# Kernel optimization log

Measured on AMD Instinct MI355X. Metric: run time of the kernel, lower is better.

## Reference

```python
import jax, jax.numpy as jnp
import numpy as np

N_DOMAINS = 8
LN_EPS = 1e-5


def setup_inputs() -> dict:
    key = jax.random.key(0)
    ks = jax.random.split(key, 4)
    N, D_IN, D_HID, D_OUT = 32768, 256, 1024, 256
    x = jax.random.normal(ks[0], (N, D_IN), dtype=jnp.float32)
    domain_types = jax.random.randint(ks[1], (N,), 0, N_DOMAINS, dtype=jnp.int32)
    # Per-domain MLP parameters (8 independent experts)
    W1 = jax.random.normal(ks[2], (N_DOMAINS, D_IN, D_HID), dtype=jnp.float32) * (1.0 / np.sqrt(D_IN))
    b1 = jnp.zeros((N_DOMAINS, D_HID), dtype=jnp.float32)
    gamma = jnp.ones((N_DOMAINS, D_HID), dtype=jnp.float32)
    beta = jnp.zeros((N_DOMAINS, D_HID), dtype=jnp.float32)
    W2 = jax.random.normal(ks[3], (N_DOMAINS, D_HID, D_OUT), dtype=jnp.float32) * (1.0 / np.sqrt(D_HID))
    b2 = jnp.zeros((N_DOMAINS, D_OUT), dtype=jnp.float32)
    return {"x": x, "domain_types": domain_types, "W1": W1, "b1": b1,
            "gamma": gamma, "beta": beta, "W2": W2, "b2": b2}


def _expert_mlp(x, W1d, b1d, gd, bd, W2d, b2d):
    # Linear -> LayerNorm -> ReLU -> (Dropout: identity at eval) -> Linear
    h = x @ W1d + b1d                       # [N, hid]
    mu = jnp.mean(h, axis=-1, keepdims=True)
    var = jnp.mean(jnp.square(h - mu), axis=-1, keepdims=True)
    h = (h - mu) * jax.lax.rsqrt(var + LN_EPS) * gd + bd
    h = jax.nn.relu(h)
    return h @ W2d + b2d                    # [N, out]


def reference(x, domain_types, W1, b1, gamma, beta, W2, b2):
    # output dim == x.shape[-1] (as in the torch code: zeros(batch, x.shape[-1]))
    out = jnp.zeros((x.shape[0], x.shape[-1]), dtype=x.dtype)
    for d in range(N_DOMAINS):  # small fixed expert loop (static MoE dispatch)
        y = _expert_mlp(x, W1[d], b1[d], gamma[d], beta[d], W2[d], b2[d])
        mask = (domain_types == d)[:, None]
        out = jnp.where(mask, y, out)
    return out
```

## Files before the change

### kernel.cpp

```cpp
#include <hip/hip_runtime.h>
#include <hip/hip_bf16.h>


#define ND 8
#define NROWS 32768
#define DIN 256
#define DHID 1024
#define DOUT 256
#define RPT 64
#define MPAD64 33280
#define NT64 520

typedef short short8 __attribute__((ext_vector_type(8)));
typedef float floatx4 __attribute__((ext_vector_type(4)));

__device__ __forceinline__ unsigned short f2bf(float f) {
    unsigned u = __builtin_bit_cast(unsigned, f);
    unsigned r = u + 0x7fff + ((u >> 16) & 1);
    return (unsigned short)(r >> 16);
}

__global__ void transpose_bf16(const float* __restrict__ in,
                               unsigned short* __restrict__ out,
                               int R, int C) {
    __shared__ float t[32][33];
    const int z = blockIdx.z;
    const int c0 = blockIdx.x * 32, r0 = blockIdx.y * 32;
    const int tx = threadIdx.x & 31, ty = threadIdx.x >> 5;
    const float* src = in + (size_t)z * R * C;
    unsigned short* dst = out + (size_t)z * R * C;
#pragma unroll
    for (int i = 0; i < 32; i += 8)
        t[ty + i][tx] = src[(size_t)(r0 + ty + i) * C + c0 + tx];
    __syncthreads();
#pragma unroll
    for (int i = 0; i < 32; i += 8)
        dst[(size_t)(c0 + ty + i) * R + r0 + tx] = f2bf(t[tx][ty + i]);
}

__global__ void zero_init(int* __restrict__ perm, int* __restrict__ cnt) {
    int i = blockIdx.x * 256 + threadIdx.x;
    if (i < MPAD64) perm[i] = -1;
    if (i < 16) cnt[i] = 0;
}

__global__ void histo(const int* __restrict__ dt, int* __restrict__ counts) {
    __shared__ int lc[ND];
    if (threadIdx.x < ND) lc[threadIdx.x] = 0;
    __syncthreads();
    int i = blockIdx.x * 256 + threadIdx.x;
    atomicAdd(&lc[dt[i]], 1);
    __syncthreads();
    if (threadIdx.x < ND) atomicAdd(&counts[threadIdx.x], lc[threadIdx.x]);
}

__global__ void make_meta(const int* __restrict__ counts, int* __restrict__ cursors,
                          int2* __restrict__ meta) {
    __shared__ int base[ND], ntc[ND];
    const int t = threadIdx.x;
    if (t == 0) {
        int off = 0;
        for (int d = 0; d < ND; d++) {
            base[d] = off;
            ntc[d] = (counts[d] + 63) >> 6;
            cursors[d] = off;
            off += ntc[d] << 6;
        }
    }
    __syncthreads();
    for (int i = t; i < NT64; i += 64) {
        int2 m = make_int2(-1, 0);
#pragma unroll
        for (int d = 0; d < ND; d++) {
            const int ti = i - (base[d] >> 6);
            if (ti >= 0 && ti < ntc[d]) m = make_int2(d, base[d] + (ti << 6));
        }
        meta[i] = m;
    }
}

__global__ __launch_bounds__(256)
void assign_pos(const int* __restrict__ dt, int* __restrict__ cursors,
                int* __restrict__ perm) {
    __shared__ int lcnt[ND];
    __shared__ int lbase[ND];
    const int tid = threadIdx.x;
    if (tid < ND) lcnt[tid] = 0;
    __syncthreads();
    const int r = blockIdx.x * 256 + tid;
    const int d = dt[r];
    const int myrank = atomicAdd(&lcnt[d], 1);
    __syncthreads();
    if (tid < ND && lcnt[tid] > 0)
        lbase[tid] = atomicAdd(&cursors[tid], lcnt[tid]);
    __syncthreads();
    perm[lbase[d] + myrank] = r;
}

__global__ __launch_bounds__(512, 2)
void fused_mlp(const float* __restrict__ x,
               const unsigned short* __restrict__ W1T,
               const float* __restrict__ b1,
               const float* __restrict__ gamma,
               const float* __restrict__ beta,
               const unsigned short* __restrict__ W2T,
               const float* __restrict__ b2,
               const int2* __restrict__ meta,
               const int* __restrict__ perm,
               float* __restrict__ out) {
    const int bid = (int)blockIdx.x;
    const int swz = (bid & 7) * (NT64 >> 3) + (bid >> 3);
    const int2 md = meta[swz];
    const int dom = md.x;
    if (dom < 0) return;
    const int m0 = md.y;

    __shared__ unsigned short Hs[RPT * DHID];
    __shared__ float red[1024];
    unsigned short* Axs = Hs;

    const int tid = threadIdx.x;
    const int lane = tid & 63;
    const int w = tid >> 6;
    const int l15 = lane & 15;
    const int q = lane >> 4;

    {
        const int row = tid >> 3;
        const int c8 = tid & 7;
        const int orig = perm[m0 + row];
        const int sw = (row & 7) << 3;
        if (orig >= 0) {
            const float4* src = (const float4*)(x + (size_t)orig * DIN);
#pragma unroll
            for (int it = 0; it < 8; ++it) {
                const int c = it * 8 + c8;
                const float4 v = src[c];
                ushort4 o;
                o.x = f2bf(v.x); o.y = f2bf(v.y); o.z = f2bf(v.z); o.w = f2bf(v.w);
                *(ushort4*)&Axs[(row * DIN + c * 4) ^ sw] = o;
            }
        } else {
            const ushort4 z = {0, 0, 0, 0};
#pragma unroll
            for (int it = 0; it < 8; ++it) {
                const int c = it * 8 + c8;
                *(ushort4*)&Axs[(row * DIN + c * 4) ^ sw] = z;
            }
        }
    }

    const int n0w = w * 128;
    const unsigned short* B1p = W1T + (size_t)dom * DHID * DIN
                              + (size_t)(n0w + l15) * DIN + q * 8;
    short8 bA[8], bB[8];
#pragma unroll
    for (int j = 0; j < 8; ++j)
        bA[j] = *(const short8*)(B1p + (size_t)j * 16 * DIN);

    __syncthreads();

    floatx4 acc[4][8];
#pragma unroll
    for (int i = 0; i < 4; ++i)
#pragma unroll
        for (int j = 0; j < 8; ++j) acc[i][j] = 0.f;

#pragma unroll
    for (int t = 0; t < 8; ++t) {
        const int k0 = t * 32;
        short8* bc = (t & 1) ? bB : bA;
        short8* bn = (t & 1) ? bA : bB;
        if (t < 7) {
#pragma unroll
            for (int j = 0; j < 8; ++j)
                bn[j] = *(const short8*)(B1p + (size_t)j * 16 * DIN + (k0 + 32));
        }
        short8 a[4];
#pragma unroll
        for (int i = 0; i < 4; ++i) {
            const int row = i * 16 + l15;
            a[i] = *(const short8*)&Axs[(row * DIN + k0 + q * 8) ^ ((row & 7) << 3)];
        }
        __builtin_amdgcn_s_setprio(1);
#pragma unroll
        for (int i = 0; i < 4; ++i)
#pragma unroll
            for (int j = 0; j < 8; ++j)
                acc[i][j] = __builtin_amdgcn_mfma_f32_16x16x32_bf16(a[i], bc[j], acc[i][j], 0, 0, 0);
        __builtin_amdgcn_s_setprio(0);
    }

    float b1v[8], gv[8], bv[8];
#pragma unroll
    for (int j = 0; j < 8; ++j) {
        const int col = n0w + j * 16 + l15;
        b1v[j] = b1[dom * DHID + col];
        gv[j]  = gamma[dom * DHID + col];
        bv[j]  = beta[dom * DHID + col];
    }
#pragma unroll
    for (int i = 0; i < 4; ++i)
#pragma unroll
        for (int j = 0; j < 8; ++j)
#pragma unroll
            for (int r = 0; r < 4; ++r) acc[i][j][r] += b1v[j];

#pragma unroll
    for (int i = 0; i < 4; ++i)
#pragma unroll
        for (int r = 0; r < 4; ++r) {
            float s = 0.f, s2 = 0.f;
#pragma unroll
            for (int j = 0; j < 8; ++j) {
                const float v = acc[i][j][r];
                s += v; s2 += v * v;
            }
#pragma unroll
            for (int o = 8; o; o >>= 1) {
                s  += __shfl_xor(s, o, 64);
                s2 += __shfl_xor(s2, o, 64);
            }
            if (l15 == 0) {
                const int row = i * 16 + q * 4 + r;
                red[w * 64 + row]       = s;
                red[512 + w * 64 + row] = s2;
            }
        }
    __syncthreads();
    if (tid < 64) {
        float s = 0.f, s2 = 0.f;
#pragma unroll
        for (int ww = 0; ww < 8; ++ww) {
            s  += red[ww * 64 + tid];
            s2 += red[512 + ww * 64 + tid];
        }
        const float mu  = s * (1.f / 1024.f);
        const float var = fmaxf(s2 * (1.f / 1024.f) - mu * mu, 0.f);
        red[tid]      = mu;
        red[64 + tid] = rsqrtf(var + 1e-5f);
    }
    __syncthreads();

#pragma unroll
    for (int i = 0; i < 4; ++i)
#pragma unroll
        for (int r = 0; r < 4; ++r) {
            const int row = i * 16 + q * 4 + r;
            const float mu   = red[row];
            const float rstd = red[64 + row];
            const int sw = (row & 7) << 3;
#pragma unroll
            for (int j = 0; j < 8; ++j) {
                const int col = n0w + j * 16 + l15;
                const float v = fmaxf((acc[i][j][r] - mu) * rstd * gv[j] + bv[j], 0.f);
                Hs[(row * DHID + col) ^ sw] = f2bf(v);
            }
        }
    __syncthreads();

    floatx4 acc2[4][2];
#pragma unroll
    for (int i = 0; i < 4; ++i) { acc2[i][0] = 0.f; acc2[i][1] = 0.f; }

    const int c0w = w * 32;
    const unsigned short* B2p = W2T + (size_t)dom * DOUT * DHID
                              + (size_t)(c0w + l15) * DHID + q * 8;
    short8 cA[2], cB[2];
#pragma unroll
    for (int jj = 0; jj < 2; ++jj)
        cA[jj] = *(const short8*)(B2p + (size_t)jj * 16 * DHID);

    for (int t = 0; t < 32; t += 2) {
        const int k0 = t * 32;
        if (t + 1 < 32) {
#pragma unroll
            for (int jj = 0; jj < 2; ++jj)
                cB[jj] = *(const short8*)(B2p + (size_t)jj * 16 * DHID + (k0 + 32));
        }
        {
            short8 a[4];
#pragma unroll
            for (int ii = 0; ii < 4; ++ii) {
                const int row = ii * 16 + l15;
                a[ii] = *(const short8*)&Hs[(row * DHID + k0 + q * 8) ^ ((row & 7) << 3)];
            }
            __builtin_amdgcn_s_setprio(1);
#pragma unroll
            for (int ii = 0; ii < 4; ++ii)
#pragma unroll
                for (int jj = 0; jj < 2; ++jj)
                    acc2[ii][jj] = __builtin_amdgcn_mfma_f32_16x16x32_bf16(a[ii], cA[jj], acc2[ii][jj], 0, 0, 0);
            __builtin_amdgcn_s_setprio(0);
        }
        if (t + 2 < 32) {
#pragma unroll
            for (int jj = 0; jj < 2; ++jj)
                cA[jj] = *(const short8*)(B2p + (size_t)jj * 16 * DHID + (k0 + 64));
        }
        {
            short8 a[4];
#pragma unroll
            for (int ii = 0; ii < 4; ++ii) {
                const int row = ii * 16 + l15;
                a[ii] = *(const short8*)&Hs[(row * DHID + k0 + 32 + q * 8) ^ ((row & 7) << 3)];
            }
            __builtin_amdgcn_s_setprio(1);
#pragma unroll
            for (int ii = 0; ii < 4; ++ii)
#pragma unroll
                for (int jj = 0; jj < 2; ++jj)
                    acc2[ii][jj] = __builtin_amdgcn_mfma_f32_16x16x32_bf16(a[ii], cB[jj], acc2[ii][jj], 0, 0, 0);
            __builtin_amdgcn_s_setprio(0);
        }
    }

    float b2v[2];
#pragma unroll
    for (int jj = 0; jj < 2; ++jj)
        b2v[jj] = b2[dom * DOUT + c0w + jj * 16 + l15];
#pragma unroll
    for (int ii = 0; ii < 4; ++ii)
#pragma unroll
        for (int r = 0; r < 4; ++r) {
            const int row = ii * 16 + q * 4 + r;
            const int orig = perm[m0 + row];
            if (orig < 0) continue;
#pragma unroll
            for (int jj = 0; jj < 2; ++jj)
                out[(size_t)orig * DOUT + c0w + jj * 16 + l15] = acc2[ii][jj][r] + b2v[jj];
        }
}

extern "C" void kernel_launch(void* const* d_in, const int* in_sizes, int n_in,
                              void* d_out, int out_size, void* d_ws, size_t ws_size,
                              hipStream_t stream) {
    const float* x = (const float*)d_in[0];
    const int* dt = (const int*)d_in[1];
    const float* W1 = (const float*)d_in[2];
    const float* b1 = (const float*)d_in[3];
    const float* gamma = (const float*)d_in[4];
    const float* beta = (const float*)d_in[5];
    const float* W2 = (const float*)d_in[6];
    const float* b2 = (const float*)d_in[7];
    float* out = (float*)d_out;

    char* ws = (char*)d_ws;
    size_t off = 0;
    auto take = [&](size_t nbytes) -> char* {
        char* p = ws + off;
        off = (off + nbytes + 255) & ~(size_t)255;
        return p;
    };
    unsigned short* W1T = (unsigned short*)take((size_t)ND * DHID * DIN * 2);
    unsigned short* W2T = (unsigned short*)take((size_t)ND * DOUT * DHID * 2);
    int* PERM = (int*)take(MPAD64 * 4);
    int* CNT  = (int*)take(64);
    int2* META = (int2*)take(NT64 * 8);
    (void)ws_size; (void)n_in; (void)in_sizes; (void)out_size;

    int* COUNTS = CNT;
    int* CURSORS = CNT + 8;

    transpose_bf16<<<dim3(DHID / 32, DIN / 32, ND), 256, 0, stream>>>(W1, W1T, DIN, DHID);
    transpose_bf16<<<dim3(DOUT / 32, DHID / 32, ND), 256, 0, stream>>>(W2, W2T, DHID, DOUT);
    zero_init<<<MPAD64 / 256, 256, 0, stream>>>(PERM, CNT);
    histo<<<NROWS / 256, 256, 0, stream>>>(dt, COUNTS);
    make_meta<<<1, 64, 0, stream>>>(COUNTS, CURSORS, META);
    assign_pos<<<NROWS / 256, 256, 0, stream>>>(dt, CURSORS, PERM);
    fused_mlp<<<NT64, 512, 0, stream>>>(x, W1T, b1, gamma, beta, W2T, b2, META, PERM, out);
}
```

Before: 235.3 us.

## Halve row tile to 32 and split hidden GEMM into two passes for occupancy

```diff
diff --git a/kernel.cpp b/kernel.cpp
--- a/kernel.cpp
+++ b/kernel.cpp
@@ -7,9 +7,9 @@
 #define DIN 256
 #define DHID 1024
 #define DOUT 256
-#define RPT 64
-#define MPAD64 33280
-#define NT64 520
+#define RPT 32
+#define MPAD32 33024
+#define NT32 1032
 
 typedef short short8 __attribute__((ext_vector_type(8)));
 typedef float floatx4 __attribute__((ext_vector_type(4)));
@@ -18,6 +18,10 @@
     unsigned u = __builtin_bit_cast(unsigned, f);
     unsigned r = u + 0x7fff + ((u >> 16) & 1);
     return (unsigned short)(r >> 16);
+}
+__device__ __forceinline__ float bf2f(unsigned short h) {
+    unsigned u = ((unsigned)h) << 16;
+    return __builtin_bit_cast(float, u);
 }
 
 __global__ void transpose_bf16(const float* __restrict__ in,
@@ -40,7 +44,7 @@
 
 __global__ void zero_init(int* __restrict__ perm, int* __restrict__ cnt) {
     int i = blockIdx.x * 256 + threadIdx.x;
-    if (i < MPAD64) perm[i] = -1;
+    if (i < MPAD32) perm[i] = -1;
     if (i < 16) cnt[i] = 0;
 }
 
@@ -62,18 +66,18 @@
         int off = 0;
         for (int d = 0; d < ND; d++) {
             base[d] = off;
-            ntc[d] = (counts[d] + 63) >> 6;
+            ntc[d] = (counts[d] + 31) >> 5;
             cursors[d] = off;
-            off += ntc[d] << 6;
-        }
-    }
-    __syncthreads();
-    for (int i = t; i < NT64; i += 64) {
+            off += ntc[d] << 5;
+        }
+    }
+    __syncthreads();
+    for (int i = t; i < NT32; i += 64) {
         int2 m = make_int2(-1, 0);
 #pragma unroll
         for (int d = 0; d < ND; d++) {
-            const int ti = i - (base[d] >> 6);
-            if (ti >= 0 && ti < ntc[d]) m = make_int2(d, base[d] + (ti << 6));
+            const int ti = i - (base[d] >> 5);
+            if (ti >= 0 && ti < ntc[d]) m = make_int2(d, base[d] + (ti << 5));
         }
         meta[i] = m;
     }
@@ -97,7 +101,7 @@
     perm[lbase[d] + myrank] = r;
 }
 
-__global__ __launch_bounds__(512, 2)
+__global__ __launch_bounds__(512, 4)
 void fused_mlp(const float* __restrict__ x,
                const unsigned short* __restrict__ W1T,
                const float* __restrict__ b1,
@@ -109,15 +113,15 @@
                const int* __restrict__ perm,
                float* __restrict__ out) {
     const int bid = (int)blockIdx.x;
-    const int swz = (bid & 7) * (NT64 >> 3) + (bid >> 3);
+    const int swz = (bid & 7) * (NT32 >> 3) + (bid >> 3);
     const int2 md = meta[swz];
     const int dom = md.x;
     if (dom < 0) return;
     const int m0 = md.y;
 
-    __shared__ unsigned short Hs[RPT * DHID];
-    __shared__ float red[1024];
-    unsigned short* Axs = Hs;
+    __shared__ __attribute__((aligned(16))) unsigned short Hs[RPT * DHID];
+    __shared__ __attribute__((aligned(16))) unsigned short Axs[RPT * DIN];
+    float* red = (float*)Axs;
 
     const int tid = threadIdx.x;
     const int lane = tid & 63;
@@ -125,16 +129,24 @@
     const int l15 = lane & 15;
     const int q = lane >> 4;
 
+    const unsigned short* W1d = W1T + (size_t)dom * DHID * DIN;
+    const unsigned short* Bp0 = W1d + (size_t)(w * 64 + l15) * DIN + q * 8;
+
+    short8 bA[4], bB[4];
+#pragma unroll
+    for (int j = 0; j < 4; ++j)
+        bA[j] = *(const short8*)(Bp0 + (size_t)j * 16 * DIN);
+
     {
-        const int row = tid >> 3;
-        const int c8 = tid & 7;
+        const int row = tid >> 4;
+        const int c16 = tid & 15;
         const int orig = perm[m0 + row];
         const int sw = (row & 7) << 3;
         if (orig >= 0) {
             const float4* src = (const float4*)(x + (size_t)orig * DIN);
 #pragma unroll
-            for (int it = 0; it < 8; ++it) {
-                const int c = it * 8 + c8;
+            for (int it = 0; it < 4; ++it) {
+                const int c = it * 16 + c16;
                 const float4 v = src[c];
                 ushort4 o;
                 o.x = f2bf(v.x); o.y = f2bf(v.y); o.z = f2bf(v.z); o.w = f2bf(v.w);
@@ -143,125 +155,109 @@
         } else {
             const ushort4 z = {0, 0, 0, 0};
 #pragma unroll
-            for (int it = 0; it < 8; ++it) {
-                const int c = it * 8 + c8;
+            for (int it = 0; it < 4; ++it) {
+                const int c = it * 16 + c16;
                 *(ushort4*)&Axs[(row * DIN + c * 4) ^ sw] = z;
             }
         }
     }
-
-    const int n0w = w * 128;
-    const unsigned short* B1p = W1T + (size_t)dom * DHID * DIN
-                              + (size_t)(n0w + l15) * DIN + q * 8;
-    short8 bA[8], bB[8];
-#pragma unroll
-    for (int j = 0; j < 8; ++j)
-        bA[j] = *(const short8*)(B1p + (size_t)j * 16 * DIN);
-
-    __syncthreads();
-
-    floatx4 acc[4][8];
-#pragma unroll
-    for (int i = 0; i < 4; ++i)
-#pragma unroll
-        for (int j = 0; j < 8; ++j) acc[i][j] = 0.f;
-
-#pragma unroll
-    for (int t = 0; t < 8; ++t) {
-        const int k0 = t * 32;
-        short8* bc = (t & 1) ? bB : bA;
-        short8* bn = (t & 1) ? bA : bB;
-        if (t < 7) {
-#pragma unroll
-            for (int j = 0; j < 8; ++j)
-                bn[j] = *(const short8*)(B1p + (size_t)j * 16 * DIN + (k0 + 32));
-        }
-        short8 a[4];
-#pragma unroll
-        for (int i = 0; i < 4; ++i) {
-            const int row = i * 16 + l15;
-            a[i] = *(const short8*)&Axs[(row * DIN + k0 + q * 8) ^ ((row & 7) << 3)];
-        }
-        __builtin_amdgcn_s_setprio(1);
-#pragma unroll
-        for (int i = 0; i < 4; ++i)
-#pragma unroll
-            for (int j = 0; j < 8; ++j)
-                acc[i][j] = __builtin_amdgcn_mfma_f32_16x16x32_bf16(a[i], bc[j], acc[i][j], 0, 0, 0);
-        __builtin_amdgcn_s_setprio(0);
-    }
-
-    float b1v[8], gv[8], bv[8];
-#pragma unroll
-    for (int j = 0; j < 8; ++j) {
-        const int col = n0w + j * 16 + l15;
-        b1v[j] = b1[dom * DHID + col];
-        gv[j]  = gamma[dom * DHID + col];
-        bv[j]  = beta[dom * DHID + col];
-    }
-#pragma unroll
-    for (int i = 0; i < 4; ++i)
-#pragma unroll
-        for (int j = 0; j < 8; ++j)
-#pragma unroll
-            for (int r = 0; r < 4; ++r) acc[i][j][r] += b1v[j];
-
-#pragma unroll
-    for (int i = 0; i < 4; ++i)
+    __syncthreads();
+
+    float sp[2][4], sp2[2][4];
+#pragma unroll
+    for (int i = 0; i < 2; ++i)
+#pragma unroll
+        for (int r = 0; r < 4; ++r) { sp[i][r] = 0.f; sp2[i][r] = 0.f; }
+
+#pragma unroll
+    for (int p = 0; p < 2; ++p) {
+        const int cb = p * 512 + w * 64;
+        const unsigned short* B1p = Bp0 + (size_t)(p * 512) * DIN;
+
+        floatx4 acc[2][4];
+#pragma unroll
+        for (int i = 0; i < 2; ++i)
+#pragma unroll
+            for (int j = 0; j < 4; ++j) acc[i][j] = 0.f;
+
+#pragma unroll
+        for (int t = 0; t < 8; ++t) {
+            const int k0 = t * 32;
+            short8* bc = (t & 1) ? bB : bA;
+            short8* bn = (t & 1) ? bA : bB;
+            if (t < 7) {
+#pragma unroll
+                for (int j = 0; j < 4; ++j)
+                    bn[j] = *(const short8*)(B1p + (size_t)j * 16 * DIN + (k0 + 32));
+            } else if (p == 0) {
+#pragma unroll
+                for (int j = 0; j < 4; ++j)
+                    bA[j] = *(const short8*)(Bp0 + (size_t)(512 + j * 16) * DIN);
+            }
+            short8 a[2];
+#pragma unroll
+            for (int i = 0; i < 2; ++i) {
+                const int row = i * 16 + l15;
+                a[i] = *(const short8*)&Axs[(row * DIN + k0 + q * 8) ^ ((row & 7) << 3)];
+            }
+            __builtin_amdgcn_s_setprio(1);
+#pragma unroll
+            for (int i = 0; i < 2; ++i)
+#pragma unroll
+                for (int j = 0; j < 4; ++j)
+                    acc[i][j] = __builtin_amdgcn_mfma_f32_16x16x32_bf16(a[i], bc[j], acc[i][j], 0, 0, 0);
+            __builtin_amdgcn_s_setprio(0);
+        }
+
+#pragma unroll
+        for (int j = 0; j < 4; ++j) {
+            const float b1v = b1[dom * DHID + cb + j * 16 + l15];
+#pragma unroll
+            for (int i = 0; i < 2; ++i)
+#pragma unroll
+                for (int r = 0; r < 4; ++r) acc[i][j][r] += b1v;
+        }
+#pragma unroll
+        for (int i = 0; i < 2; ++i)
+#pragma unroll
+            for (int r = 0; r < 4; ++r) {
+                float s = 0.f, s2 = 0.f;
+#pragma unroll
+                for (int j = 0; j < 4; ++j) {
+                    const float v = acc[i][j][r];
+                    s += v; s2 += v * v;
+                }
+                sp[i][r] += s; sp2[i][r] += s2;
+            }
+#pragma unroll
+        for (int i = 0; i < 2; ++i)
+#pragma unroll
+            for (int r = 0; r < 4; ++r) {
+                const int row = i * 16 + q * 4 + r;
+                const int sw = (row & 7) << 3;
+#pragma unroll
+                for (int j = 0; j < 4; ++j)
+                    Hs[(row * DHID + cb + j * 16 + l15) ^ sw] = f2bf(acc[i][j][r]);
+            }
+    }
+
+    __syncthreads();
+
+#pragma unroll
+    for (int i = 0; i < 2; ++i)
 #pragma unroll
         for (int r = 0; r < 4; ++r) {
-            float s = 0.f, s2 = 0.f;
-#pragma unroll
-            for (int j = 0; j < 8; ++j) {
-                const float v = acc[i][j][r];
-                s += v; s2 += v * v;
-            }
 #pragma unroll
             for (int o = 8; o; o >>= 1) {
-                s  += __shfl_xor(s, o, 64);
-                s2 += __shfl_xor(s2, o, 64);
+                sp[i][r]  += __shfl_xor(sp[i][r], o, 64);
+                sp2[i][r] += __shfl_xor(sp2[i][r], o, 64);
             }
             if (l15 == 0) {
                 const int row = i * 16 + q * 4 + r;
-                red[w * 64 + row]       = s;
-                red[512 + w * 64 + row] = s2;
-            }
-        }
-    __syncthreads();
-    if (tid < 64) {
-        float s = 0.f, s2 = 0.f;
-#pragma unroll
-        for (int ww = 0; ww < 8; ++ww) {
-            s  += red[ww * 64 + tid];
-            s2 += red[512 + ww * 64 + tid];
-        }
-        const float mu  = s * (1.f / 1024.f);
-        const float var = fmaxf(s2 * (1.f / 1024.f) - mu * mu, 0.f);
-        red[tid]      = mu;
-        red[64 + tid] = rsqrtf(var + 1e-5f);
-    }
-    __syncthreads();
-
-#pragma unroll
-    for (int i = 0; i < 4; ++i)
-#pragma unroll
-        for (int r = 0; r < 4; ++r) {
-            const int row = i * 16 + q * 4 + r;
-            const float mu   = red[row];
-            const float rstd = red[64 + row];
-            const int sw = (row & 7) << 3;
-#pragma unroll
-            for (int j = 0; j < 8; ++j) {
-                const int col = n0w + j * 16 + l15;
-                const float v = fmaxf((acc[i][j][r] - mu) * rstd * gv[j] + bv[j], 0.f);
-                Hs[(row * DHID + col) ^ sw] = f2bf(v);
-            }
-        }
-    __syncthreads();
-
-    floatx4 acc2[4][2];
-#pragma unroll
-    for (int i = 0; i < 4; ++i) { acc2[i][0] = 0.f; acc2[i][1] = 0.f; }
+                red[w * 32 + row]       = sp[i][r];
+                red[256 + w * 32 + row] = sp2[i][r];
+            }
+        }
 
     const int c0w = w * 32;
     const unsigned short* B2p = W2T + (size_t)dom * DOUT * DHID
@@ -271,6 +267,55 @@
     for (int jj = 0; jj < 2; ++jj)
         cA[jj] = *(const short8*)(B2p + (size_t)jj * 16 * DHID);
 
+    __syncthreads();
+    if (tid < 32) {
+        float s = 0.f, s2 = 0.f;
+#pragma unroll
+        for (int ww = 0; ww < 8; ++ww) {
+            s  += red[ww * 32 + tid];
+            s2 += red[256 + ww * 32 + tid];
+        }
+        const float mu  = s * (1.f / 1024.f);
+        const float var = fmaxf(s2 * (1.f / 1024.f) - mu * mu, 0.f);
+        red[512 + tid] = mu;
+        red[544 + tid] = rsqrtf(var + 1e-5f);
+    }
+    __syncthreads();
+
+    {
+        const float* gdp = gamma + dom * DHID;
+        const float* bdp = beta + dom * DHID;
+#pragma unroll
+        for (int kq = 0; kq < 8; ++kq) {
+            const int ch = tid + kq * 512;
+            const int row = ch >> 7;
+            const int c0 = (ch & 127) * 8;
+            const int idx = (row * DHID + c0) ^ ((row & 7) << 3);
+            short8 hv = *(short8*)&Hs[idx];
+            const float mu   = red[512 + row];
+            const float rstd = red[544 + row];
+            const float4 g0 = *(const float4*)(gdp + c0);
+            const float4 g1 = *(const float4*)(gdp + c0 + 4);
+            const float4 be0 = *(const float4*)(bdp + c0);
+            const float4 be1 = *(const float4*)(bdp + c0 + 4);
+            short8 o;
+            o[0] = (short)f2bf(fmaxf((bf2f((unsigned short)hv[0]) - mu) * rstd * g0.x + be0.x, 0.f));
+            o[1] = (short)f2bf(fmaxf((bf2f((unsigned short)hv[1]) - mu) * rstd * g0.y + be0.y, 0.f));
+            o[2] = (short)f2bf(fmaxf((bf2f((unsigned short)hv[2]) - mu) * rstd * g0.z + be0.z, 0.f));
+            o[3] = (short)f2bf(fmaxf((bf2f((unsigned short)hv[3]) - mu) * rstd * g0.w + be0.w, 0.f));
+            o[4] = (short)f2bf(fmaxf((bf2f((unsigned short)hv[4]) - mu) * rstd * g1.x + be1.x, 0.f));
+            o[5] = (short)f2bf(fmaxf((bf2f((unsigned short)hv[5]) - mu) * rstd * g1.y + be1.y, 0.f));
+            o[6] = (short)f2bf(fmaxf((bf2f((unsigned short)hv[6]) - mu) * rstd * g1.z + be1.z, 0.f));
+            o[7] = (short)f2bf(fmaxf((bf2f((unsigned short)hv[7]) - mu) * rstd * g1.w + be1.w, 0.f));
+            *(short8*)&Hs[idx] = o;
+        }
+    }
+    __syncthreads();
+
+    floatx4 acc2[2][2];
+#pragma unroll
+    for (int ii = 0; ii < 2; ++ii) { acc2[ii][0] = 0.f; acc2[ii][1] = 0.f; }
+
     for (int t = 0; t < 32; t += 2) {
         const int k0 = t * 32;
         if (t + 1 < 32) {
@@ -279,15 +324,15 @@
                 cB[jj] = *(const short8*)(B2p + (size_t)jj * 16 * DHID + (k0 + 32));
         }
         {
-            short8 a[4];
-#pragma unroll
-            for (int ii = 0; ii < 4; ++ii) {
+            short8 a[2];
+#pragma unroll
+            for (int ii = 0; ii < 2; ++ii) {
                 const int row = ii * 16 + l15;
                 a[ii] = *(const short8*)&Hs[(row * DHID + k0 + q * 8) ^ ((row & 7) << 3)];
             }
             __builtin_amdgcn_s_setprio(1);
 #pragma unroll
-            for (int ii = 0; ii < 4; ++ii)
+            for (int ii = 0; ii < 2; ++ii)
 #pragma unroll
                 for (int jj = 0; jj < 2; ++jj)
                     acc2[ii][jj] = __builtin_amdgcn_mfma_f32_16x16x32_bf16(a[ii], cA[jj], acc2[ii][jj], 0, 0, 0);
@@ -299,15 +344,15 @@
                 cA[jj] = *(const short8*)(B2p + (size_t)jj * 16 * DHID + (k0 + 64));
         }
         {
-            short8 a[4];
-#pragma unroll
-            for (int ii = 0; ii < 4; ++ii) {
+            short8 a[2];
+#pragma unroll
+            for (int ii = 0; ii < 2; ++ii) {
                 const int row = ii * 16 + l15;
                 a[ii] = *(const short8*)&Hs[(row * DHID + k0 + 32 + q * 8) ^ ((row & 7) << 3)];
             }
             __builtin_amdgcn_s_setprio(1);
 #pragma unroll
-            for (int ii = 0; ii < 4; ++ii)
+            for (int ii = 0; ii < 2; ++ii)
 #pragma unroll
                 for (int jj = 0; jj < 2; ++jj)
                     acc2[ii][jj] = __builtin_amdgcn_mfma_f32_16x16x32_bf16(a[ii], cB[jj], acc2[ii][jj], 0, 0, 0);
@@ -320,7 +365,7 @@
     for (int jj = 0; jj < 2; ++jj)
         b2v[jj] = b2[dom * DOUT + c0w + jj * 16 + l15];
 #pragma unroll
-    for (int ii = 0; ii < 4; ++ii)
+    for (int ii = 0; ii < 2; ++ii)
 #pragma unroll
         for (int r = 0; r < 4; ++r) {
             const int row = ii * 16 + q * 4 + r;
@@ -354,9 +399,9 @@
     };
     unsigned short* W1T = (unsigned short*)take((size_t)ND * DHID * DIN * 2);
     unsigned short* W2T = (unsigned short*)take((size_t)ND * DOUT * DHID * 2);
-    int* PERM = (int*)take(MPAD64 * 4);
+    int* PERM = (int*)take(MPAD32 * 4);
     int* CNT  = (int*)take(64);
-    int2* META = (int2*)take(NT64 * 8);
+    int2* META = (int2*)take(NT32 * 8);
     (void)ws_size; (void)n_in; (void)in_sizes; (void)out_size;
 
     int* COUNTS = CNT;
@@ -364,9 +409,9 @@
 
     transpose_bf16<<<dim3(DHID / 32, DIN / 32, ND), 256, 0, stream>>>(W1, W1T, DIN, DHID);
     transpose_bf16<<<dim3(DOUT / 32, DHID / 32, ND), 256, 0, stream>>>(W2, W2T, DHID, DOUT);
-    zero_init<<<MPAD64 / 256, 256, 0, stream>>>(PERM, CNT);
+    zero_init<<<(MPAD32 + 255) / 256, 256, 0, stream>>>(PERM, CNT);
     histo<<<NROWS / 256, 256, 0, stream>>>(dt, COUNTS);
     make_meta<<<1, 64, 0, stream>>>(COUNTS, CURSORS, META);
     assign_pos<<<NROWS / 256, 256, 0, stream>>>(dt, CURSORS, PERM);
-    fused_mlp<<<NT64, 512, 0, stream>>>(x, W1T, b1, gamma, beta, W2T, b2, META, PERM, out);
-}
+    fused_mlp<<<NT32, 512, 0, stream>>>(x, W1T, b1, gamma, beta, W2T, b2, META, PERM, out);
+}
```

Measured after the change: 280.4 us. +19.2%, slower.
